# Performance work log

Hardware: AMD Instinct MI355X
Metric: run time of the kernel (lower is better)

Reference implementation:

```python
import jax, jax.numpy as jnp
import numpy as np

N_NODES = 25000
N_EDGES = 300000
N_GRAPHS = 256
EMB_DIM = 92
HID = 256
EDGE_F = 4


def _lin(key, fan_in, fan_out):
    kw, kb = jax.random.split(key)
    s = 1.0 / np.sqrt(fan_in)
    W = jax.random.uniform(kw, (fan_in, fan_out), jnp.float32, -s, s)
    b = jax.random.uniform(kb, (fan_out,), jnp.float32, -s, s)
    return W, b


def setup_inputs() -> dict:
    key = jax.random.key(0)
    ks = jax.random.split(key, 32)
    x_atoms = jax.random.randint(ks[0], (N_NODES,), 0, 119)
    edge_index = jax.random.randint(ks[1], (2, N_EDGES), 0, N_NODES)
    edge_attr = jax.random.normal(ks[2], (N_EDGES, EDGE_F), jnp.float32)
    batch = jnp.sort(jax.random.randint(ks[3], (N_NODES,), 0, N_GRAPHS))
    emb = jax.random.normal(ks[4], (119, EMB_DIM), jnp.float32)
    emb = emb.at[0].set(0.0)  # padding_idx=0
    # layer 0: in=92, out=256
    ew1_0, eb1_0 = _lin(ks[5], EDGE_F, EMB_DIM)
    ew2_0, eb2_0 = _lin(ks[6], EMB_DIM, EMB_DIM)
    nw_0, nb_0 = _lin(ks[7], EMB_DIM, HID)
    # layers 1..3 stacked: in=out=256
    ew1, eb1, ew2, eb2, nw, nb = [], [], [], [], [], []
    for i in range(3):
        a, b = _lin(ks[8 + 3 * i], EDGE_F, HID)
        c, d = _lin(ks[9 + 3 * i], HID, HID)
        e, f = _lin(ks[10 + 3 * i], HID, HID)
        ew1.append(a); eb1.append(b); ew2.append(c); eb2.append(d); nw.append(e); nb.append(f)
    ew1 = jnp.stack(ew1); eb1 = jnp.stack(eb1); ew2 = jnp.stack(ew2)
    eb2 = jnp.stack(eb2); nw = jnp.stack(nw); nb = jnp.stack(nb)
    rw1, rb1 = _lin(ks[20], HID, HID)
    rw2, rb2 = _lin(ks[21], HID, HID // 2)
    rw3, rb3 = _lin(ks[22], HID // 2, 1)
    return dict(x_atoms=x_atoms, edge_index=edge_index, edge_attr=edge_attr, batch=batch,
                emb=emb, ew1_0=ew1_0, eb1_0=eb1_0, ew2_0=ew2_0, eb2_0=eb2_0, nw_0=nw_0, nb_0=nb_0,
                ew1=ew1, eb1=eb1, ew2=ew2, eb2=eb2, nw=nw, nb=nb,
                rw1=rw1, rb1=rb1, rw2=rw2, rb2=rb2, rw3=rw3, rb3=rb3)


def _conv(x, src, dst, edge_attr, ew1, eb1, ew2, eb2, nw, nb):
    # edge MLP: Linear -> Softplus -> Linear
    ee = jax.nn.softplus(edge_attr @ ew1 + eb1) @ ew2 + eb2  # [E, C]
    msg = ee * x[src]                                        # gather + multiply
    agg = jax.ops.segment_sum(msg, dst, num_segments=x.shape[0])  # scatter-add
    return jax.nn.softplus(agg @ nw + nb)


def reference(x_atoms, edge_index, edge_attr, batch, emb,
              ew1_0, eb1_0, ew2_0, eb2_0, nw_0, nb_0,
              ew1, eb1, ew2, eb2, nw, nb,
              rw1, rb1, rw2, rb2, rw3, rb3):
    src, dst = edge_index[0], edge_index[1]  # PyG: x_j = x[src], aggregate at dst
    x = emb[x_atoms]  # [N, 92]
    x = _conv(x, src, dst, edge_attr, ew1_0, eb1_0, ew2_0, eb2_0, nw_0, nb_0)
    for i in range(3):
        x = _conv(x, src, dst, edge_attr, ew1[i], eb1[i], ew2[i], eb2[i], nw[i], nb[i])
    # global mean pool
    sums = jax.ops.segment_sum(x, batch, num_segments=N_GRAPHS)
    cnts = jax.ops.segment_sum(jnp.ones((x.shape[0],), x.dtype), batch, num_segments=N_GRAPHS)
    g = sums / jnp.maximum(cnts, 1.0)[:, None]  # [G, 256]
    h = jax.nn.softplus(g @ rw1 + rb1)          # dropout is identity in eval mode
    h = jax.nn.softplus(h @ rw2 + rb2)
    out = (h @ rw3 + rb3).squeeze(-1)           # [G]
    return out
```

## Files before the change

### kernel.cpp

```cpp
#include <hip/hip_runtime.h>
#include <math.h>

#define N_NODES  25000
#define N_EDGES  300000
#define N_GRAPHS 256
#define EMB_DIM  92
#define HID      256

typedef short bf16x8 __attribute__((ext_vector_type(8)));
typedef float f32x4  __attribute__((ext_vector_type(4)));

__device__ __forceinline__ float softplusf(float x){
    return fmaxf(x, 0.0f) + __logf(1.0f + __expf(-fabsf(x)));
}
__device__ __forceinline__ unsigned short f2bf(float f){
    unsigned int u = __float_as_uint(f);
    unsigned int r = (u + 0x7FFFu + ((u >> 16) & 1u)) >> 16;
    return (unsigned short)r;
}
__device__ __forceinline__ unsigned short f2bf_trunc(float f){
    return (unsigned short)(__float_as_uint(f) >> 16);
}
__device__ __forceinline__ float bf2f(unsigned short b){
    return __uint_as_float(((unsigned int)b) << 16);
}
__device__ __forceinline__ void split_bf(float h, unsigned short& hi, unsigned short& lo){
    const unsigned int u = __float_as_uint(h);
    hi = (unsigned short)(u >> 16);
    const float r = h - __uint_as_float(u & 0xFFFF0000u);
    lo = (unsigned short)(__float_as_uint(r) >> 16);
}
__device__ __forceinline__ int xcd_window(int nwin){
    const int per = (nwin + 7) >> 3;
    const int win = (blockIdx.x & 7) * per + (blockIdx.x >> 3);
    return (win < nwin) ? win : -1;
}

__global__ void gather_emb_kernel(const int* __restrict__ atoms,
                                  const float* __restrict__ emb,
                                  float* __restrict__ x)
{
    const int n = blockIdx.x;
    const int c = threadIdx.x;
    if (c < EMB_DIM){
        const int a = atoms[n];
        x[(size_t)n*EMB_DIM + c] = emb[(size_t)a*EMB_DIM + c];
    }
}

__global__ __launch_bounds__(256) void hist_kernel(const int* __restrict__ dst, int* __restrict__ hist){
    const int e = blockIdx.x*256 + threadIdx.x;
    if (e < N_EDGES) atomicAdd(&hist[dst[e]], 1);
}

__global__ __launch_bounds__(1024) void scan_kernel(const int* __restrict__ hist, int* __restrict__ cursor){
    __shared__ int chunk[1024];
    const int t = threadIdx.x;
    const int base = t*25;
    int local[25];
    int s = 0;
    #pragma unroll
    for (int i=0;i<25;i++){
        const int idx = base+i;
        const int v = (idx < N_NODES) ? hist[idx] : 0;
        local[i] = s; s += v;
    }
    chunk[t] = s;
    __syncthreads();
    for (int off=1; off<1024; off<<=1){
        int v = (t >= off) ? chunk[t-off] : 0;
        __syncthreads();
        chunk[t] += v;
        __syncthreads();
    }
    const int pre = (t > 0) ? chunk[t-1] : 0;
    #pragma unroll
    for (int i=0;i<25;i++){
        const int idx = base+i;
        if (idx < N_NODES) cursor[idx] = pre + local[i];
    }
}

__global__ __launch_bounds__(256) void scatter_kernel(const int* __restrict__ src, const int* __restrict__ dst,
                                                      const float* __restrict__ ea,
                                                      int* __restrict__ cursor,
                                                      int* __restrict__ src_s, int* __restrict__ dst_s,
                                                      float* __restrict__ ea_s){
    const int e = blockIdx.x*256 + threadIdx.x;
    if (e < N_EDGES){
        const int d = dst[e];
        const int pos = atomicAdd(&cursor[d], 1);
        src_s[pos] = src[e];
        dst_s[pos] = d;
        const float4 a = *(const float4*)(ea + (size_t)e*4);
        *(float4*)(ea_s + (size_t)pos*4) = a;
    }
}

__global__ __launch_bounds__(256) void pack_w_kernel(const float* __restrict__ w,
                                                     unsigned short* __restrict__ whi,
                                                     unsigned short* __restrict__ wlo)
{
    const int f     = blockIdx.x;
    const int layer = f >> 7;
    const int rem   = f & 127;
    const int ntile = rem >> 3;
    const int k8    = rem & 7;
    for (int i = threadIdx.x; i < 512; i += 256){
        const int lane = i >> 3, j = i & 7;
        const int k = k8*32 + (lane >> 4)*8 + j;
        const int n = ntile*16 + (lane & 15);
        const float v = w[(size_t)layer*HID*HID + (size_t)k*HID + n];
        const unsigned short hb = f2bf(v);
        whi[(size_t)f*512 + i] = hb;
        wlo[(size_t)f*512 + i] = f2bf(v - bf2f(hb));
    }
}

__global__ __launch_bounds__(256) void pack_w_pad_kernel(const float* __restrict__ w,
                                                         int Kin, int Nin, int ldn,
                                                         unsigned short* __restrict__ whi,
                                                         unsigned short* __restrict__ wlo)
{
    const int f  = blockIdx.x;
    const int k8 = f % 3;
    const int ntile = f / 3;
    for (int i = threadIdx.x; i < 512; i += 256){
        const int lane = i >> 3, j = i & 7;
        const int k = k8*32 + (lane >> 4)*8 + j;
        const int n = ntile*16 + (lane & 15);
        float v = 0.0f;
        if (k < Kin && n < Nin) v = w[(size_t)k*ldn + n];
        const unsigned short hb = f2bf(v);
        whi[(size_t)f*512 + i] = hb;
        wlo[(size_t)f*512 + i] = f2bf(v - bf2f(hb));
    }
}

__global__ __launch_bounds__(256, 4) void edge_conv92_mfma_kernel(
    const int* __restrict__ src_s, const int* __restrict__ dst_s,
    const float* __restrict__ ea_s,
    const float* __restrict__ w1, const float* __restrict__ b1,
    const unsigned short* __restrict__ whi, const unsigned short* __restrict__ wlo,
    const float* __restrict__ b2,
    const float* __restrict__ x92, float* __restrict__ agg92)
{
    constexpr int C = EMB_DIM;
    constexpr int KP = 96;
    constexpr int LDA = 104;
    constexpr int EPB = 64;
    constexpr int NWIN = (N_EDGES + EPB - 1) / EPB;
    __shared__ unsigned short aHi[EPB][LDA];
    __shared__ float eaS[EPB][4];
    __shared__ int   srcS[EPB];
    __shared__ int   dstS[EPB];

    const int win = xcd_window(NWIN);
    if (win < 0) return;
    const int e0  = win * EPB;
    const int tid = threadIdx.x;

    {
        const int e = tid >> 2, comp = tid & 3;
        const int eid = min(e0 + e, N_EDGES-1);
        eaS[e][comp] = ea_s[(size_t)eid*4 + comp];
        if (tid < EPB){
            const int eid2 = min(e0 + tid, N_EDGES-1);
            srcS[tid] = src_s[eid2];
            dstS[tid] = dst_s[eid2];
        }
    }
    __syncthreads();

    for (int idx = tid; idx < EPB*KP; idx += 256){
        const int e = idx / KP, k = idx - e*KP;
        float h = 0.0f;
        if (k < C){
            const float4 a = *(const float4*)&eaS[e][0];
            h = softplusf(fmaf(a.x, w1[k], fmaf(a.y, w1[C+k],
                          fmaf(a.z, w1[2*C+k], fmaf(a.w, w1[3*C+k], b1[k])))));
        }
        const int row = (e>>5)*32 + ((e>>2)&1)*16 + ((e>>3)&3)*4 + (e&3);
        aHi[row][k] = f2bf_trunc(h);
    }
    __syncthreads();

    const int lane = tid & 63, wv = tid >> 6;
    const int quad = lane >> 4, fcol = lane & 15;
    const int mpair = wv >> 1;
    const int ngrp  = wv & 1;

    f32x4 acc[2][3];
    #pragma unroll
    for (int m=0;m<2;m++)
        #pragma unroll
        for (int t=0;t<3;t++)
            #pragma unroll
            for (int j=0;j<4;j++) acc[m][t][j] = 0.0f;

    for (int k8=0;k8<3;k8++){
        bf16x8 ah[2];
        #pragma unroll
        for (int m=0;m<2;m++)
            ah[m] = *(const bf16x8*)(&aHi[mpair*32 + m*16 + fcol][0] + k8*32 + quad*8);
        #pragma unroll
        for (int t=0;t<3;t++){
            const int fi = (ngrp*3 + t)*3 + k8;
            const bf16x8 bh = *(const bf16x8*)(whi + (size_t)fi*512 + lane*8);
            const bf16x8 bl = *(const bf16x8*)(wlo + (size_t)fi*512 + lane*8);
            #pragma unroll
            for (int m=0;m<2;m++){
                acc[m][t] = __builtin_amdgcn_mfma_f32_16x16x32_bf16(ah[m], bh, acc[m][t], 0, 0, 0);
                acc[m][t] = __builtin_amdgcn_mfma_f32_16x16x32_bf16(ah[m], bl, acc[m][t], 0, 0, 0);
            }
        }
    }

    int   ncol[3]; float bb[3];
    #pragma unroll
    for (int t=0;t<3;t++){
        ncol[t] = (ngrp*3 + t)*16 + fcol;
        bb[t] = (ncol[t] < C) ? b2[ncol[t]] : 0.0f;
    }

    const int ebase = mpair*32 + quad*8;
    float xv[8][3];
    #pragma unroll
    for (int j=0;j<8;j++){
        const int s = srcS[ebase + j];
        const bool valid = (e0 + ebase + j) < N_EDGES;
        #pragma unroll
        for (int t=0;t<3;t++)
            xv[j][t] = (valid && ncol[t] < C) ? x92[(size_t)s*C + ncol[t]] : 0.0f;
    }

    int dprev = dstS[ebase];
    float run[3] = {0.f,0.f,0.f};
    #pragma unroll
    for (int j=0;j<8;j++){
        const int d = dstS[ebase + j];
        if (d != dprev){
            #pragma unroll
            for (int t=0;t<3;t++){
                if (ncol[t] < C) atomicAdd(&agg92[(size_t)dprev*C + ncol[t]], run[t]);
                run[t] = 0.0f;
            }
            dprev = d;
        }
        #pragma unroll
        for (int t=0;t<3;t++)
            run[t] += (acc[j>>2][t][j&3] + bb[t]) * xv[j][t];
    }
    #pragma unroll
    for (int t=0;t<3;t++)
        if (ncol[t] < C) atomicAdd(&agg92[(size_t)dprev*C + ncol[t]], run[t]);
}

__global__ __launch_bounds__(256) void node_update92_mfma_kernel(
    const float* __restrict__ agg92,
    const unsigned short* __restrict__ whi, const unsigned short* __restrict__ wlo,
    const float* __restrict__ b, float* __restrict__ xout)
{
    constexpr int C = EMB_DIM;
    constexpr int KP = 96;
    constexpr int LDA = 104;
    __shared__ unsigned short aHi[16][LDA];
    __shared__ unsigned short aLo[16][LDA];

    const int n0  = blockIdx.x * 16;
    const int tid = threadIdx.x;

    for (int idx = tid; idx < 16*KP; idx += 256){
        const int i = idx / KP, k = idx - i*KP;
        const int node = n0 + i;
        float v = 0.0f;
        if (k < C && node < N_NODES) v = agg92[(size_t)node*C + k];
        unsigned short hb, lb;
        split_bf(v, hb, lb);
        aHi[i][k] = hb;
        aLo[i][k] = lb;
    }
    __syncthreads();

    const int lane = tid & 63, wv = tid >> 6;
    const int quad = lane >> 4, fcol = lane & 15;

    f32x4 acc[4];
    #pragma unroll
    for (int t=0;t<4;t++)
        #pragma unroll
        for (int j=0;j<4;j++) acc[t][j] = 0.0f;

    const unsigned short* aHrow = &aHi[fcol][0];
    const unsigned short* aLrow = &aLo[fcol][0];

    for (int k8=0;k8<3;k8++){
        const bf16x8 ah = *(const bf16x8*)(aHrow + k8*32 + quad*8);
        const bf16x8 al = *(const bf16x8*)(aLrow + k8*32 + quad*8);
        #pragma unroll
        for (int t=0;t<4;t++){
            const int fi = (wv*4 + t)*3 + k8;
            const bf16x8 bh = *(const bf16x8*)(whi + (size_t)fi*512 + lane*8);
            const bf16x8 bl = *(const bf16x8*)(wlo + (size_t)fi*512 + lane*8);
            acc[t] = __builtin_amdgcn_mfma_f32_16x16x32_bf16(ah, bh, acc[t], 0, 0, 0);
            acc[t] = __builtin_amdgcn_mfma_f32_16x16x32_bf16(ah, bl, acc[t], 0, 0, 0);
            acc[t] = __builtin_amdgcn_mfma_f32_16x16x32_bf16(al, bh, acc[t], 0, 0, 0);
        }
    }

    #pragma unroll
    for (int i=0;i<4;i++){
        const int node = n0 + quad*4 + i;
        if (node < N_NODES){
            #pragma unroll
            for (int t=0;t<4;t++){
                const int n = (wv*4 + t)*16 + fcol;
                xout[(size_t)node*HID + n] = softplusf(acc[t][i] + b[n]);
            }
        }
    }
}

__global__ __launch_bounds__(512, 6) void edge_conv256_mfma_kernel(
    const int* __restrict__ src_s, const int* __restrict__ dst_s,
    const float* __restrict__ ea_s,
    const float* __restrict__ w1, const float* __restrict__ b1,
    const unsigned short* __restrict__ whi, const unsigned short* __restrict__ wlo,
    const float* __restrict__ b2,
    const float* __restrict__ x, float* __restrict__ agg)
{
    constexpr int C = HID;
    constexpr int LDA = C + 8;
    constexpr int EPB = 64;
    constexpr int NWIN = (N_EDGES + EPB - 1) / EPB;
    __shared__ unsigned short aHi[EPB][LDA];
    __shared__ float eaS[EPB][4];
    __shared__ int   srcS[EPB];
    __shared__ int   dstS[EPB];

    const int win = xcd_window(NWIN);
    if (win < 0) return;
    const int e0  = win * EPB;
    const int tid = threadIdx.x;

    if (tid < 256){
        const int e = tid >> 2, comp = tid & 3;
        const int eid = min(e0 + e, N_EDGES-1);
        eaS[e][comp] = ea_s[(size_t)eid*4 + comp];
    } else if (tid < 320){
        const int e = tid - 256;
        srcS[e] = src_s[min(e0 + e, N_EDGES-1)];
    } else if (tid < 384){
        const int e = tid - 320;
        dstS[e] = dst_s[min(e0 + e, N_EDGES-1)];
    }
    __syncthreads();

    {
        const int k = tid & 255;
        const int g = tid >> 8;
        const float w10 = w1[k], w11 = w1[C+k], w12 = w1[2*C+k], w13 = w1[3*C+k];
        const float bk  = b1[k];
        #pragma unroll
        for (int ii=0; ii<32; ii++){
            const int e = g*32 + ii;
            const float4 a = *(const float4*)&eaS[e][0];
            const float v = fmaf(a.x,w10,fmaf(a.y,w11,fmaf(a.z,w12,fmaf(a.w,w13,bk))));
            const int q = e >> 4, j = e & 15;
            aHi[(j>>2)*16 + q*4 + (j&3)][k] = f2bf_trunc(softplusf(v));
        }
    }
    __syncthreads();

    const int lane = tid & 63, wv = tid >> 6;
    const int quad = lane >> 4, fcol = lane & 15;

    f32x4 acc[4][2];
    #pragma unroll
    for (int m=0;m<4;m++)
        #pragma unroll
        for (int t=0;t<2;t++)
            #pragma unroll
            for (int j=0;j<4;j++) acc[m][t][j] = 0.0f;

    for (int k8=0;k8<8;k8++){
        bf16x8 ah[4];
        #pragma unroll
        for (int m=0;m<4;m++)
            ah[m] = *(const bf16x8*)(&aHi[m*16 + fcol][0] + k8*32 + quad*8);
        #pragma unroll
        for (int t=0;t<2;t++){
            const int fi = (wv*2 + t)*8 + k8;
            const bf16x8 bh = *(const bf16x8*)(whi + (size_t)fi*512 + lane*8);
            const bf16x8 bl = *(const bf16x8*)(wlo + (size_t)fi*512 + lane*8);
            #pragma unroll
            for (int m=0;m<4;m++){
                acc[m][t] = __builtin_amdgcn_mfma_f32_16x16x32_bf16(ah[m], bh, acc[m][t], 0, 0, 0);
                acc[m][t] = __builtin_amdgcn_mfma_f32_16x16x32_bf16(ah[m], bl, acc[m][t], 0, 0, 0);
            }
        }
    }

    float bb[2];
    #pragma unroll
    for (int t=0;t<2;t++) bb[t] = b2[(wv*2 + t)*16 + fcol];

    const int ebase = quad*16;
    float xv[16][2];
    #pragma unroll
    for (int j=0;j<16;j++){
        const int s = srcS[ebase + j];
        const bool valid = (e0 + ebase + j) < N_EDGES;
        #pragma unroll
        for (int t=0;t<2;t++)
            xv[j][t] = valid ? x[(size_t)s*C + (wv*2 + t)*16 + fcol] : 0.0f;
    }

    int dprev = dstS[ebase];
    float run[2] = {0.f,0.f};
    #pragma unroll
    for (int j=0;j<16;j++){
        const int d = dstS[ebase + j];
        if (d != dprev){
            #pragma unroll
            for (int t=0;t<2;t++){
                atomicAdd(&agg[(size_t)dprev*C + (wv*2 + t)*16 + fcol], run[t]);
                run[t] = 0.0f;
            }
            dprev = d;
        }
        #pragma unroll
        for (int t=0;t<2;t++)
            run[t] += (acc[j>>2][t][j&3] + bb[t]) * xv[j][t];
    }
    #pragma unroll
    for (int t=0;t<2;t++)
        atomicAdd(&agg[(size_t)dprev*C + (wv*2 + t)*16 + fcol], run[t]);
}

__global__ __launch_bounds__(256) void node_update_mfma_kernel(
    float* __restrict__ agg,
    const unsigned short* __restrict__ whi, const unsigned short* __restrict__ wlo,
    const float* __restrict__ b, float* __restrict__ xout, int zero_agg)
{
    constexpr int C = HID;
    constexpr int LDA = C + 8;
    __shared__ unsigned short aHi[16][LDA];
    __shared__ unsigned short aLo[16][LDA];

    const int n0  = blockIdx.x * 16;
    const int tid = threadIdx.x;

    #pragma unroll
    for (int it=0; it<16; it++){
        const int node = n0 + it;
        float v = 0.0f;
        if (node < N_NODES){
            v = agg[(size_t)node*C + tid];
            if (zero_agg) agg[(size_t)node*C + tid] = 0.0f;
        }
        unsigned short hb, lb;
        split_bf(v, hb, lb);
        aHi[it][tid] = hb;
        aLo[it][tid] = lb;
    }
    __syncthreads();

    const int lane = tid & 63, wv = tid >> 6;
    const int quad = lane >> 4, fcol = lane & 15;

    f32x4 acc[4];
    #pragma unroll
    for (int t=0;t<4;t++)
        #pragma unroll
        for (int j=0;j<4;j++) acc[t][j] = 0.0f;

    const unsigned short* aHrow = &aHi[fcol][0];
    const unsigned short* aLrow = &aLo[fcol][0];

    for (int k8=0;k8<8;k8++){
        const bf16x8 ah = *(const bf16x8*)(aHrow + k8*32 + quad*8);
        const bf16x8 al = *(const bf16x8*)(aLrow + k8*32 + quad*8);
        #pragma unroll
        for (int t=0;t<4;t++){
            const int fi = (wv*4 + t)*8 + k8;
            const bf16x8 bh = *(const bf16x8*)(whi + (size_t)fi*512 + lane*8);
            const bf16x8 bl = *(const bf16x8*)(wlo + (size_t)fi*512 + lane*8);
            acc[t] = __builtin_amdgcn_mfma_f32_16x16x32_bf16(ah, bh, acc[t], 0, 0, 0);
            acc[t] = __builtin_amdgcn_mfma_f32_16x16x32_bf16(ah, bl, acc[t], 0, 0, 0);
            acc[t] = __builtin_amdgcn_mfma_f32_16x16x32_bf16(al, bh, acc[t], 0, 0, 0);
        }
    }

    #pragma unroll
    for (int i=0;i<4;i++){
        const int node = n0 + quad*4 + i;
        if (node < N_NODES){
            #pragma unroll
            for (int t=0;t<4;t++){
                const int n = (wv*4 + t)*16 + fcol;
                xout[(size_t)node*C + n] = softplusf(acc[t][i] + b[n]);
            }
        }
    }
}

__global__ __launch_bounds__(256) void pool_kernel(
    const float* __restrict__ x, const int* __restrict__ batch,
    float* __restrict__ sums, float* __restrict__ cnts)
{
    constexpr int NPB = 32;
    const int n0 = blockIdx.x * NPB;
    const int c  = threadIdx.x;
    int gprev = batch[n0];
    float run = 0.0f, crun = 0.0f;
    for (int i=0;i<NPB;i++){
        const int n = n0 + i;
        if (n >= N_NODES) break;
        const int g = batch[n];
        if (g != gprev){
            atomicAdd(&sums[(size_t)gprev*HID + c], run);
            if (c == 0) atomicAdd(&cnts[gprev], crun);
            run = 0.0f; crun = 0.0f; gprev = g;
        }
        run  += x[(size_t)n*HID + c];
        crun += 1.0f;
    }
    atomicAdd(&sums[(size_t)gprev*HID + c], run);
    if (c == 0) atomicAdd(&cnts[gprev], crun);
}

__global__ __launch_bounds__(256) void readout_kernel(
    const float* __restrict__ sums, const float* __restrict__ cnts,
    const float* __restrict__ rw1, const float* __restrict__ rb1,
    const float* __restrict__ rw2, const float* __restrict__ rb2,
    const float* __restrict__ rw3, const float* __restrict__ rb3,
    float* __restrict__ out)
{
    __shared__ float g[HID];
    __shared__ float h[HID];
    __shared__ float h2[HID/2];
    __shared__ float red[256];
    const int gi = blockIdx.x;
    const int t  = threadIdx.x;
    const float cnt = fmaxf(cnts[gi], 1.0f);
    g[t] = sums[(size_t)gi*HID + t] / cnt;
    __syncthreads();
    float acc = rb1[t];
    for (int k=0;k<HID;k++) acc = fmaf(g[k], rw1[(size_t)k*HID + t], acc);
    h[t] = softplusf(acc);
    __syncthreads();
    if (t < HID/2){
        float a2 = rb2[t];
        for (int k=0;k<HID;k++) a2 = fmaf(h[k], rw2[(size_t)k*(HID/2) + t], a2);
        h2[t] = softplusf(a2);
    }
    __syncthreads();
    red[t] = (t < HID/2) ? h2[t]*rw3[t] : 0.0f;
    __syncthreads();
    for (int s2=128; s2>0; s2>>=1){
        if (t < s2) red[t] += red[t+s2];
        __syncthreads();
    }
    if (t == 0) out[gi] = red[0] + rb3[0];
}

extern "C" void kernel_launch(void* const* d_in, const int* in_sizes, int n_in,
                              void* d_out, int out_size, void* d_ws, size_t ws_size,
                              hipStream_t stream)
{
    const int*   x_atoms = (const int*)d_in[0];
    const int*   eidx    = (const int*)d_in[1];
    const int*   src     = eidx;
    const int*   dst     = eidx + N_EDGES;
    const float* ea      = (const float*)d_in[2];
    const int*   batch   = (const int*)d_in[3];
    const float* emb     = (const float*)d_in[4];
    const float* ew1_0   = (const float*)d_in[5];
    const float* eb1_0   = (const float*)d_in[6];
    const float* ew2_0   = (const float*)d_in[7];
    const float* eb2_0   = (const float*)d_in[8];
    const float* nw_0    = (const float*)d_in[9];
    const float* nb_0    = (const float*)d_in[10];
    const float* ew1     = (const float*)d_in[11];
    const float* eb1     = (const float*)d_in[12];
    const float* ew2     = (const float*)d_in[13];
    const float* eb2     = (const float*)d_in[14];
    const float* nw      = (const float*)d_in[15];
    const float* nb      = (const float*)d_in[16];
    const float* rw1     = (const float*)d_in[17];
    const float* rb1     = (const float*)d_in[18];
    const float* rw2     = (const float*)d_in[19];
    const float* rb2     = (const float*)d_in[20];
    const float* rw3     = (const float*)d_in[21];
    const float* rb3     = (const float*)d_in[22];
    float* out = (float*)d_out;

    float* x    = (float*)d_ws;
    float* agg  = x   + (size_t)N_NODES*HID;
    float* sums = agg + (size_t)N_NODES*HID;
    float* cnts = sums + (size_t)N_GRAPHS*HID;
    unsigned short* whi  = (unsigned short*)(cnts + N_GRAPHS);
    unsigned short* wlo  = whi  + (size_t)3*128*512;
    unsigned short* nwhi = wlo  + (size_t)3*128*512;
    unsigned short* nwlo = nwhi + (size_t)3*128*512;
    unsigned short* w92hi  = nwlo  + (size_t)3*128*512;
    unsigned short* w92lo  = w92hi + (size_t)18*512;
    unsigned short* nw92hi = w92lo + (size_t)18*512;
    unsigned short* nw92lo = nw92hi + (size_t)48*512;
    float* ea_s = (float*)(nw92lo + (size_t)48*512);
    int* hist   = (int*)(ea_s + (size_t)N_EDGES*4);
    int* cursor = hist   + N_NODES;
    int* src_s  = cursor + N_NODES;
    int* dst_s  = src_s  + N_EDGES;

    hipMemsetAsync(hist, 0, N_NODES*sizeof(int), stream);
    hipLaunchKernelGGL(hist_kernel, dim3((N_EDGES+255)/256), dim3(256), 0, stream, dst, hist);
    hipLaunchKernelGGL(scan_kernel, dim3(1), dim3(1024), 0, stream, hist, cursor);
    hipLaunchKernelGGL(scatter_kernel, dim3((N_EDGES+255)/256), dim3(256), 0, stream,
                       src, dst, ea, cursor, src_s, dst_s, ea_s);

    hipLaunchKernelGGL(pack_w_kernel, dim3(384), dim3(256), 0, stream, ew2, whi, wlo);
    hipLaunchKernelGGL(pack_w_kernel, dim3(384), dim3(256), 0, stream, nw, nwhi, nwlo);
    hipLaunchKernelGGL(pack_w_pad_kernel, dim3(18), dim3(256), 0, stream, ew2_0, EMB_DIM, EMB_DIM, EMB_DIM, w92hi, w92lo);
    hipLaunchKernelGGL(pack_w_pad_kernel, dim3(48), dim3(256), 0, stream, nw_0, EMB_DIM, HID, HID, nw92hi, nw92lo);

    const int NWIN64 = (N_EDGES + 63) / 64;

    hipLaunchKernelGGL(gather_emb_kernel, dim3(N_NODES), dim3(128), 0, stream, x_atoms, emb, x);
    hipMemsetAsync(agg, 0, (size_t)N_NODES*EMB_DIM*sizeof(float), stream);
    hipLaunchKernelGGL(edge_conv92_mfma_kernel, dim3((NWIN64+7)/8*8), dim3(256), 0, stream,
                       src_s, dst_s, ea_s, ew1_0, eb1_0, w92hi, w92lo, eb2_0, x, agg);
    hipLaunchKernelGGL(node_update92_mfma_kernel, dim3((N_NODES+15)/16), dim3(256), 0, stream,
                       agg, nw92hi, nw92lo, nb_0, x);

    hipMemsetAsync(agg, 0, (size_t)N_NODES*HID*sizeof(float), stream);

    for (int i=0;i<3;i++){
        hipLaunchKernelGGL(edge_conv256_mfma_kernel, dim3((NWIN64+7)/8*8), dim3(512), 0, stream,
                           src_s, dst_s, ea_s,
                           ew1 + (size_t)i*4*HID, eb1 + (size_t)i*HID,
                           whi + (size_t)i*128*512, wlo + (size_t)i*128*512,
                           eb2 + (size_t)i*HID,
                           x, agg);
        hipLaunchKernelGGL(node_update_mfma_kernel, dim3((N_NODES+15)/16), dim3(256), 0, stream,
                           agg, nwhi + (size_t)i*128*512, nwlo + (size_t)i*128*512,
                           nb + (size_t)i*HID, x, (i < 2) ? 1 : 0);
    }

    hipMemsetAsync(sums, 0, ((size_t)N_GRAPHS*HID + N_GRAPHS)*sizeof(float), stream);
    hipLaunchKernelGGL(pool_kernel, dim3((N_NODES+31)/32), dim3(256), 0, stream, x, batch, sums, cnts);
    hipLaunchKernelGGL(readout_kernel, dim3(N_GRAPHS), dim3(256), 0, stream,
                       sums, cnts, rw1, rb1, rw2, rb2, rw3, rb3, out);
}
```

Before: 703.1 us.

## Drop bf16 low-part MFMA in edge conv, merge weight packing, precompute graph counts

```diff
diff --git a/kernel.cpp b/kernel.cpp
--- a/kernel.cpp
+++ b/kernel.cpp
@@ -48,9 +48,11 @@
     }
 }
 
-__global__ __launch_bounds__(256) void hist_kernel(const int* __restrict__ dst, int* __restrict__ hist){
+__global__ __launch_bounds__(256) void hist_kernel(const int* __restrict__ dst, int* __restrict__ hist,
+                                                   const int* __restrict__ batch, int* __restrict__ gcnt){
     const int e = blockIdx.x*256 + threadIdx.x;
     if (e < N_EDGES) atomicAdd(&hist[dst[e]], 1);
+    if (e < N_NODES) atomicAdd(&gcnt[batch[e]], 1);
 }
 
 __global__ __launch_bounds__(1024) void scan_kernel(const int* __restrict__ hist, int* __restrict__ cursor){
@@ -97,11 +99,7 @@
     }
 }
 
-__global__ __launch_bounds__(256) void pack_w_kernel(const float* __restrict__ w,
-                                                     unsigned short* __restrict__ whi,
-                                                     unsigned short* __restrict__ wlo)
-{
-    const int f     = blockIdx.x;
+__device__ __forceinline__ void pack256_dev(const float* w, unsigned short* whi, unsigned short* wlo, int f){
     const int layer = f >> 7;
     const int rem   = f & 127;
     const int ntile = rem >> 3;
@@ -116,13 +114,8 @@
         wlo[(size_t)f*512 + i] = f2bf(v - bf2f(hb));
     }
 }
-
-__global__ __launch_bounds__(256) void pack_w_pad_kernel(const float* __restrict__ w,
-                                                         int Kin, int Nin, int ldn,
-                                                         unsigned short* __restrict__ whi,
-                                                         unsigned short* __restrict__ wlo)
-{
-    const int f  = blockIdx.x;
+__device__ __forceinline__ void packpad_dev(const float* w, int Kin, int Nin, int ldn,
+                                            unsigned short* whi, unsigned short* wlo, int f){
     const int k8 = f % 3;
     const int ntile = f / 3;
     for (int i = threadIdx.x; i < 512; i += 256){
@@ -136,6 +129,20 @@
         wlo[(size_t)f*512 + i] = f2bf(v - bf2f(hb));
     }
 }
+__global__ __launch_bounds__(256) void pack_all_kernel(
+    const float* __restrict__ ew2, const float* __restrict__ nw,
+    const float* __restrict__ ew2_0, const float* __restrict__ nw_0,
+    unsigned short* whi, unsigned short* wlo,
+    unsigned short* nwhi, unsigned short* nwlo,
+    unsigned short* w92hi, unsigned short* w92lo,
+    unsigned short* nw92hi, unsigned short* nw92lo)
+{
+    const int b = blockIdx.x;
+    if (b < 384)      pack256_dev(ew2, whi, wlo, b);
+    else if (b < 768) pack256_dev(nw, nwhi, nwlo, b-384);
+    else if (b < 786) packpad_dev(ew2_0, EMB_DIM, EMB_DIM, EMB_DIM, w92hi, w92lo, b-768);
+    else              packpad_dev(nw_0, EMB_DIM, HID, HID, nw92hi, nw92lo, b-786);
+}
 
 __global__ __launch_bounds__(256, 4) void edge_conv92_mfma_kernel(
     const int* __restrict__ src_s, const int* __restrict__ dst_s,
@@ -325,7 +332,7 @@
     const int* __restrict__ src_s, const int* __restrict__ dst_s,
     const float* __restrict__ ea_s,
     const float* __restrict__ w1, const float* __restrict__ b1,
-    const unsigned short* __restrict__ whi, const unsigned short* __restrict__ wlo,
+    const unsigned short* __restrict__ whi,
     const float* __restrict__ b2,
     const float* __restrict__ x, float* __restrict__ agg)
 {
@@ -357,17 +364,21 @@
     __syncthreads();
 
     {
-        const int k = tid & 255;
-        const int g = tid >> 8;
-        const float w10 = w1[k], w11 = w1[C+k], w12 = w1[2*C+k], w13 = w1[3*C+k];
-        const float bk  = b1[k];
-        #pragma unroll
-        for (int ii=0; ii<32; ii++){
-            const int e = g*32 + ii;
+        const int k2 = (tid & 127) * 2;
+        const int g  = tid >> 7;
+        const float wa0 = w1[k2],   wa1 = w1[C+k2],   wa2 = w1[2*C+k2],   wa3 = w1[3*C+k2];
+        const float wb0 = w1[k2+1], wb1 = w1[C+k2+1], wb2 = w1[2*C+k2+1], wb3 = w1[3*C+k2+1];
+        const float bk0 = b1[k2], bk1 = b1[k2+1];
+        #pragma unroll
+        for (int ii=0; ii<16; ii++){
+            const int e = g*16 + ii;
             const float4 a = *(const float4*)&eaS[e][0];
-            const float v = fmaf(a.x,w10,fmaf(a.y,w11,fmaf(a.z,w12,fmaf(a.w,w13,bk))));
+            const float v0 = fmaf(a.x,wa0,fmaf(a.y,wa1,fmaf(a.z,wa2,fmaf(a.w,wa3,bk0))));
+            const float v1 = fmaf(a.x,wb0,fmaf(a.y,wb1,fmaf(a.z,wb2,fmaf(a.w,wb3,bk1))));
+            const unsigned int packed = (unsigned int)f2bf_trunc(softplusf(v0))
+                                      | ((unsigned int)f2bf_trunc(softplusf(v1)) << 16);
             const int q = e >> 4, j = e & 15;
-            aHi[(j>>2)*16 + q*4 + (j&3)][k] = f2bf_trunc(softplusf(v));
+            *(unsigned int*)&aHi[(j>>2)*16 + q*4 + (j&3)][k2] = packed;
         }
     }
     __syncthreads();
@@ -392,12 +403,9 @@
         for (int t=0;t<2;t++){
             const int fi = (wv*2 + t)*8 + k8;
             const bf16x8 bh = *(const bf16x8*)(whi + (size_t)fi*512 + lane*8);
-            const bf16x8 bl = *(const bf16x8*)(wlo + (size_t)fi*512 + lane*8);
-            #pragma unroll
-            for (int m=0;m<4;m++){
+            #pragma unroll
+            for (int m=0;m<4;m++)
                 acc[m][t] = __builtin_amdgcn_mfma_f32_16x16x32_bf16(ah[m], bh, acc[m][t], 0, 0, 0);
-                acc[m][t] = __builtin_amdgcn_mfma_f32_16x16x32_bf16(ah[m], bl, acc[m][t], 0, 0, 0);
-            }
         }
     }
 
@@ -507,31 +515,28 @@
 
 __global__ __launch_bounds__(256) void pool_kernel(
     const float* __restrict__ x, const int* __restrict__ batch,
-    float* __restrict__ sums, float* __restrict__ cnts)
+    float* __restrict__ sums)
 {
     constexpr int NPB = 32;
     const int n0 = blockIdx.x * NPB;
     const int c  = threadIdx.x;
     int gprev = batch[n0];
-    float run = 0.0f, crun = 0.0f;
+    float run = 0.0f;
     for (int i=0;i<NPB;i++){
         const int n = n0 + i;
         if (n >= N_NODES) break;
         const int g = batch[n];
         if (g != gprev){
             atomicAdd(&sums[(size_t)gprev*HID + c], run);
-            if (c == 0) atomicAdd(&cnts[gprev], crun);
-            run = 0.0f; crun = 0.0f; gprev = g;
-        }
-        run  += x[(size_t)n*HID + c];
-        crun += 1.0f;
+            run = 0.0f; gprev = g;
+        }
+        run += x[(size_t)n*HID + c];
     }
     atomicAdd(&sums[(size_t)gprev*HID + c], run);
-    if (c == 0) atomicAdd(&cnts[gprev], crun);
 }
 
 __global__ __launch_bounds__(256) void readout_kernel(
-    const float* __restrict__ sums, const float* __restrict__ cnts,
+    const float* __restrict__ sums, const int* __restrict__ gcnt,
     const float* __restrict__ rw1, const float* __restrict__ rb1,
     const float* __restrict__ rw2, const float* __restrict__ rb2,
     const float* __restrict__ rw3, const float* __restrict__ rb3,
@@ -543,7 +548,7 @@
     __shared__ float red[256];
     const int gi = blockIdx.x;
     const int t  = threadIdx.x;
-    const float cnt = fmaxf(cnts[gi], 1.0f);
+    const float cnt = fmaxf((float)gcnt[gi], 1.0f);
     g[t] = sums[(size_t)gi*HID + t] / cnt;
     __syncthreads();
     float acc = rb1[t];
@@ -599,8 +604,7 @@
     float* x    = (float*)d_ws;
     float* agg  = x   + (size_t)N_NODES*HID;
     float* sums = agg + (size_t)N_NODES*HID;
-    float* cnts = sums + (size_t)N_GRAPHS*HID;
-    unsigned short* whi  = (unsigned short*)(cnts + N_GRAPHS);
+    unsigned short* whi  = (unsigned short*)(sums + (size_t)N_GRAPHS*HID);
     unsigned short* wlo  = whi  + (size_t)3*128*512;
     unsigned short* nwhi = wlo  + (size_t)3*128*512;
     unsigned short* nwlo = nwhi + (size_t)3*128*512;
@@ -610,20 +614,20 @@
     unsigned short* nw92lo = nw92hi + (size_t)48*512;
     float* ea_s = (float*)(nw92lo + (size_t)48*512);
     int* hist   = (int*)(ea_s + (size_t)N_EDGES*4);
-    int* cursor = hist   + N_NODES;
+    int* gcnt   = hist   + N_NODES;
+    int* cursor = gcnt   + N_GRAPHS;
     int* src_s  = cursor + N_NODES;
     int* dst_s  = src_s  + N_EDGES;
 
-    hipMemsetAsync(hist, 0, N_NODES*sizeof(int), stream);
-    hipLaunchKernelGGL(hist_kernel, dim3((N_EDGES+255)/256), dim3(256), 0, stream, dst, hist);
+    hipMemsetAsync(hist, 0, (N_NODES + N_GRAPHS)*sizeof(int), stream);
+    hipLaunchKernelGGL(hist_kernel, dim3((N_EDGES+255)/256), dim3(256), 0, stream, dst, hist, batch, gcnt);
     hipLaunchKernelGGL(scan_kernel, dim3(1), dim3(1024), 0, stream, hist, cursor);
     hipLaunchKernelGGL(scatter_kernel, dim3((N_EDGES+255)/256), dim3(256), 0, stream,
                        src, dst, ea, cursor, src_s, dst_s, ea_s);
 
-    hipLaunchKernelGGL(pack_w_kernel, dim3(384), dim3(256), 0, stream, ew2, whi, wlo);
-    hipLaunchKernelGGL(pack_w_kernel, dim3(384), dim3(256), 0, stream, nw, nwhi, nwlo);
-    hipLaunchKernelGGL(pack_w_pad_kernel, dim3(18), dim3(256), 0, stream, ew2_0, EMB_DIM, EMB_DIM, EMB_DIM, w92hi, w92lo);
-    hipLaunchKernelGGL(pack_w_pad_kernel, dim3(48), dim3(256), 0, stream, nw_0, EMB_DIM, HID, HID, nw92hi, nw92lo);
+    hipLaunchKernelGGL(pack_all_kernel, dim3(834), dim3(256), 0, stream,
+                       ew2, nw, ew2_0, nw_0,
+                       whi, wlo, nwhi, nwlo, w92hi, w92lo, nw92hi, nw92lo);
 
     const int NWIN64 = (N_EDGES + 63) / 64;
 
@@ -640,7 +644,7 @@
         hipLaunchKernelGGL(edge_conv256_mfma_kernel, dim3((NWIN64+7)/8*8), dim3(512), 0, stream,
                            src_s, dst_s, ea_s,
                            ew1 + (size_t)i*4*HID, eb1 + (size_t)i*HID,
-                           whi + (size_t)i*128*512, wlo + (size_t)i*128*512,
+                           whi + (size_t)i*128*512,
                            eb2 + (size_t)i*HID,
                            x, agg);
         hipLaunchKernelGGL(node_update_mfma_kernel, dim3((N_NODES+15)/16), dim3(256), 0, stream,
@@ -648,8 +652,8 @@
                            nb + (size_t)i*HID, x, (i < 2) ? 1 : 0);
     }
 
-    hipMemsetAsync(sums, 0, ((size_t)N_GRAPHS*HID + N_GRAPHS)*sizeof(float), stream);
-    hipLaunchKernelGGL(pool_kernel, dim3((N_NODES+31)/32), dim3(256), 0, stream, x, batch, sums, cnts);
+    hipMemsetAsync(sums, 0, (size_t)N_GRAPHS*HID*sizeof(float), stream);
+    hipLaunchKernelGGL(pool_kernel, dim3((N_NODES+31)/32), dim3(256), 0, stream, x, batch, sums);
     hipLaunchKernelGGL(readout_kernel, dim3(N_GRAPHS), dim3(256), 0, stream,
-                       sums, cnts, rw1, rb1, rw2, rb2, rw3, rb3, out);
-}
+                       sums, gcnt, rw1, rb1, rw2, rb2, rw3, rb3, out);
+}
```

New measurement: 656.7 us. 1.07x faster.
